# Optimization experiments

Measured on AMD Instinct MI355X. Metric: run time of the kernel, lower is better.

The kernel has to match this reference:

```python
import jax, jax.numpy as jnp
import numpy as np

BLOCK_SIZE = 32
BLOCK_COUNTS = 16
B, N, H, D = 4, 1024, 8, 64
LENGTHS = np.array([1024, 768, 512, 896], dtype=np.int64)


def setup_inputs() -> dict:
    key = jax.random.key(0)
    ks = jax.random.split(key, 8)
    offsets = np.concatenate([[0], np.cumsum(LENGTHS)]).astype(np.int32)
    mask = np.zeros((B, N), dtype=bool)
    for b in range(B):
        mask[b, : int(LENGTHS[b])] = True
    gather_idx = np.nonzero(mask.reshape(-1))[0].astype(np.int32)
    m = jnp.asarray(mask)[:, :, None, None].astype(jnp.float32)
    padded_q = jax.random.normal(ks[0], (B, N, H, D), jnp.float32) * m
    padded_k = jax.random.normal(ks[1], (B, N, H, D), jnp.float32) * m
    padded_v = jax.random.normal(ks[2], (B, N, H, D), jnp.float32) * m
    gidx = jnp.asarray(gather_idx)
    jagged_q = padded_q.reshape(B * N, H, D)[gidx]
    jagged_k = padded_k.reshape(B * N, H, D)[gidx]
    jagged_v = padded_v.reshape(B * N, H, D)[gidx]
    jagged_u = jax.random.normal(ks[3], (int(gidx.shape[0]), H, D), jnp.float32)
    gate_w = jax.random.normal(ks[4], (H, D, 3), jnp.float32) * 0.1
    return {"jagged_q": jagged_q, "jagged_k": jagged_k, "jagged_v": jagged_v,
            "jagged_u": jagged_u, "padded_q": padded_q, "padded_k": padded_k,
            "padded_v": padded_v, "x_offsets": jnp.asarray(offsets),
            "gate_w": gate_w, "padding_mask": jnp.asarray(mask),
            "gather_idx": gidx}


def _forward(jagged_q, jagged_k, jagged_v, padded_q, padded_k, padded_v,
             x_offsets, gate_w, gather_idx):
    scale = D ** -0.5
    nb = N // BLOCK_SIZE                                   # N is a multiple of BLOCK_SIZE (pad_len=0)
    S = min(BLOCK_COUNTS, nb)
    lengths = x_offsets[1:] - x_offsets[:-1]               # [B]
    cmp_len = (lengths + BLOCK_SIZE - 1) // BLOCK_SIZE     # [B] valid compressed blocks per seq
    pos = jnp.arange(N)
    blk = jnp.arange(nb)
    q_blk = pos // BLOCK_SIZE

    # scatter jagged tokens back to dense padded layout (zeros at padding) --
    # the Triton kernels read q/k/v from the jagged tensors.
    def to_dense(j):
        return jnp.zeros((B * N, H, D), j.dtype).at[gather_idx].set(j).reshape(B, N, H, D)
    qd, kd, vd = to_dense(jagged_q), to_dense(jagged_k), to_dense(jagged_v)

    # gates: per-token/per-head sigmoid linear gate from padded_q -> (g_cmp, g_slc, g_swa)
    gates = jax.nn.sigmoid(jnp.einsum('bnhd,hdg->bnhg', padded_q, gate_w))
    g_cmp, g_slc = gates[..., 0], gates[..., 1]            # g_swa unused by this module

    # compressed (block-mean) keys / values  [B, nb, H, D]
    k_cmp = padded_k.reshape(B, nb, BLOCK_SIZE, H, D).mean(axis=2)
    v_cmp = padded_v.reshape(B, nb, BLOCK_SIZE, H, D).mean(axis=2)

    # ---- compressed branch: SiLU attention over block-mean keys ----
    s_cmp = jnp.einsum('bqhd,bkhd->bqhk', qd, k_cmp) * scale          # [B,N,H,nb]
    mask_cmp = (q_blk[:, None] >= blk[None, :])[None, :, None, :] & \
               (blk[None, None, None, :] < cmp_len[:, None, None, None])
    p_cmp = jnp.where(mask_cmp, jax.nn.silu(s_cmp), 0.0)
    o_cmp = jnp.einsum('bqhk,bkhd->bqhd', p_cmp, v_cmp) * g_cmp[..., None]

    # ---- block selection: causal top-k over compressed scores ----
    s_sel = jnp.einsum('bqhd,bkhd->bhqk', padded_q, k_cmp) * scale    # [B,H,N,nb]
    causal_blk = (q_blk[:, None] >= blk[None, :])[None, None]
    _, top_idx = jax.lax.top_k(jnp.where(causal_blk, s_sel, -jnp.inf), S)  # [B,H,N,S]
    top_idx = jnp.where(top_idx > q_blk[None, None, :, None], -1, top_idx)
    top_idx = top_idx.transpose(0, 2, 1, 3)                           # [B,N,H,S]

    # ---- selected branch: SiLU attention restricted to selected blocks ----
    blk_sel = jnp.any(top_idx[..., None] == blk, axis=-2)             # [B,N,H,nb] (-1 matches nothing)
    key_sel = jnp.repeat(blk_sel, BLOCK_SIZE, axis=-1)                # [B,N,H,N]
    mask_slc = key_sel & (pos[:, None] >= pos[None, :])[None, :, None, :]
    s_slc = jnp.einsum('bqhd,bkhd->bqhk', qd, kd) * scale             # [B,N,H,N]
    p_slc = jnp.where(mask_slc, jax.nn.silu(s_slc), 0.0)
    o_slc = jnp.einsum('bqhk,bkhd->bqhd', p_slc, vd) * g_slc[..., None]

    # jagged output: gather valid tokens
    return (o_cmp + o_slc).reshape(B * N, H, D)[gather_idx]


def reference(jagged_q, jagged_k, jagged_v, jagged_u, padded_q, padded_k,
              padded_v, x_offsets, gate_w, padding_mask, gather_idx):
    return _forward(jagged_q, jagged_k, jagged_v, padded_q, padded_k,
                    padded_v, x_offsets, gate_w, gather_idx)
```

## Files before the change

kernel.cpp:

```cpp
#include <hip/hip_runtime.h>
#include <math.h>
#include <stdint.h>

#define BB 4
#define NN 1024
#define HH 8
#define DD 64
#define BS 32
#define NB 32
#define SS 16

typedef __attribute__((ext_vector_type(8)))  short bf16x8;
typedef __attribute__((ext_vector_type(16))) float f32x16;
typedef __attribute__((ext_vector_type(2)))  int   int2v;

union FragU { bf16x8 h; uint32_t u[4]; };

#define ZERO16 {0.f,0.f,0.f,0.f,0.f,0.f,0.f,0.f,0.f,0.f,0.f,0.f,0.f,0.f,0.f,0.f}

__device__ __forceinline__ uint32_t cvt_pk_bf16(float lo, float hi) {
    uint32_t r;
    asm("v_cvt_pk_bf16_f32 %0, %1, %2" : "=v"(r) : "v"(lo), "v"(hi));
    return r;
}

__device__ __forceinline__ float silu_f(float x) {
    return __fdividef(x, 1.f + __expf(-x));
}

__global__ void cmp_mean_kernel(const float* __restrict__ pk,
                                const float* __restrict__ pv,
                                float* __restrict__ kc,
                                float* __restrict__ vc) {
    int idx = blockIdx.x * 4 + (threadIdx.x >> 6);
    int d = threadIdx.x & 63;
    int h = idx & 7;
    int blk = (idx >> 3) & 31;
    int b = idx >> 8;
    size_t base = (((size_t)b * NN + (size_t)blk * BS) * HH + h) * DD + d;
    float ks = 0.f, vs = 0.f;
    #pragma unroll
    for (int j = 0; j < BS; ++j) {
        ks += pk[base + (size_t)j * HH * DD];
        vs += pv[base + (size_t)j * HH * DD];
    }
    kc[(size_t)idx * DD + d] = ks * (1.f / BS);
    vc[(size_t)idx * DD + d] = vs * (1.f / BS);
}

__global__ __launch_bounds__(256, 3) void bsa_mfma_kernel(
    const float* __restrict__ pq, const float* __restrict__ pk,
    const float* __restrict__ pv, const float* __restrict__ kc,
    const float* __restrict__ vc, const float* __restrict__ gw,
    const int* __restrict__ xoff, float* __restrict__ out)
{
    __shared__ float qlds[32][64];
    __shared__ __align__(16) uint16_t pcmp[32][40];
    __shared__ uint32_t selmask[32];
    __shared__ float gateC[32], gateS[32];
    __shared__ float olds[5][32][64];

    const int tid = threadIdx.x;
    const int lane = tid & 63;
    const int w = tid >> 6;
    const int l31 = lane & 31;
    const int hi = lane >> 5;

    const int bid = blockIdx.x;
    const int t_id = (bid & 7) * 128 + (bid >> 3);
    const int qb = t_id & 31;
    const int h = (t_id >> 5) & 7;
    const int b = t_id >> 8;

    const int off0 = xoff[b];
    const int len = xoff[b + 1] - off0;
    if (qb * BS >= len) return;

    {
        int q = tid >> 3, part = (tid & 7) * 8;
        const float* src = pq + (((size_t)(b * NN + qb * BS + q)) * HH + h) * DD + part;
        *(float4*)&qlds[q][part] = *(const float4*)src;
        *(float4*)&qlds[q][part + 4] = *(const float4*)(src + 4);
    }

    FragU qf[4];
    {
        const float* qrow = pq + (((size_t)(b * NN + qb * BS + l31)) * HH + h) * DD;
        #pragma unroll
        for (int t = 0; t < 4; ++t) {
            const float* qp = qrow + t * 16 + hi * 8;
            float4 x = *(const float4*)qp;
            float4 y = *(const float4*)(qp + 4);
            qf[t].u[0] = cvt_pk_bf16(x.x, x.y);
            qf[t].u[1] = cvt_pk_bf16(x.z, x.w);
            qf[t].u[2] = cvt_pk_bf16(y.x, y.y);
            qf[t].u[3] = cvt_pk_bf16(y.z, y.w);
        }
    }

    float4 kcv[8];
    {
        const float* kcrow = kc + (((size_t)(b * NB + l31)) * HH + h) * DD + hi * 32;
        #pragma unroll
        for (int i = 0; i < 8; ++i) kcv[i] = *(const float4*)(kcrow + i * 4);
    }

    __syncthreads();

    for (int j = 0; j < 8; ++j) {
        int q = w * 8 + j;
        const float* qv = qlds[q];
        const float* qh = qv + hi * 32;
        float part = 0.f;
        #pragma unroll
        for (int i = 0; i < 8; ++i) {
            float4 qq = *(const float4*)(qh + i * 4);
            part += qq.x * kcv[i].x + qq.y * kcv[i].y + qq.z * kcv[i].z + qq.w * kcv[i].w;
        }
        float s = (part + __shfl_xor(part, 32)) * 0.125f;
        float p = (l31 <= qb) ? silu_f(s) : 0.f;
        if (lane < 32) {
            uint32_t fb = __float_as_uint(p);
            uint16_t bp = (uint16_t)((fb + 0x7fffu + ((fb >> 16) & 1u)) >> 16);
            pcmp[q][l31] = bp;
        }
        uint32_t m;
        if (qb >= SS) {
            float vsel = (l31 <= qb) ? s : -INFINITY;
            int rank = 0;
            #pragma unroll
            for (int off = 1; off < 32; ++off) {
                float o = __shfl_xor(vsel, off);
                int oi = l31 ^ off;
                rank += (o > vsel || (o == vsel && oi < l31)) ? 1 : 0;
            }
            m = (uint32_t)(__ballot(rank < SS) & 0xffffffffu);
        } else {
            m = (1u << (qb + 1)) - 1u;
        }
        if (lane == 0) selmask[q] = m;
        float qd = qv[lane];
        float g0 = qd * gw[(h * DD + lane) * 3 + 0];
        float g1 = qd * gw[(h * DD + lane) * 3 + 1];
        #pragma unroll
        for (int off = 32; off; off >>= 1) {
            g0 += __shfl_xor(g0, off);
            g1 += __shfl_xor(g1, off);
        }
        if (lane == 0) {
            gateC[q] = __frcp_rn(1.f + __expf(-g0));
            gateS[q] = __frcp_rn(1.f + __expf(-g1));
        }
    }

    __syncthreads();

    const uint32_t mymask = selmask[l31];
    f32x16 accO0 = ZERO16, accO1 = ZERO16;

    if (w == 3) {
        f32x16 c0 = ZERO16, c1 = ZERO16;
        #pragma unroll
        for (int s = 0; s < 2; ++s) {
            FragU pa;
            pa.h = *(const bf16x8*)&pcmp[l31][s * 16 + hi * 8];
            const float* vbase = vc + (((size_t)(b * NB + s * 16 + hi * 8)) * HH + h) * DD + l31;
            #pragma unroll
            for (int dh = 0; dh < 2; ++dh) {
                FragU vb;
                #pragma unroll
                for (int jj = 0; jj < 4; ++jj) {
                    float a = vbase[(2 * jj) * 512 + dh * 32];
                    float c = vbase[(2 * jj + 1) * 512 + dh * 32];
                    vb.u[jj] = cvt_pk_bf16(a, c);
                }
                if (dh == 0) c0 = __builtin_amdgcn_mfma_f32_32x32x16_bf16(pa.h, vb.h, c0, 0, 0, 0);
                else         c1 = __builtin_amdgcn_mfma_f32_32x32x16_bf16(pa.h, vb.h, c1, 0, 0, 0);
            }
        }
        #pragma unroll
        for (int r = 0; r < 16; ++r) {
            int q = (r & 3) + 8 * (r >> 2) + 4 * hi;
            olds[4][q][l31] = c0[r];
            olds[4][q][32 + l31] = c1[r];
        }
    }

    const int qpos = qb * BS + l31;
    for (int kb = w; kb <= qb; kb += 4) {
        f32x16 accS = ZERO16;
        const float* krow = pk + (((size_t)(b * NN + kb * BS + l31)) * HH + h) * DD;
        #pragma unroll
        for (int t = 0; t < 4; ++t) {
            const float* kp = krow + t * 16 + hi * 8;
            float4 x = *(const float4*)kp;
            float4 y = *(const float4*)(kp + 4);
            FragU kf;
            kf.u[0] = cvt_pk_bf16(x.x, x.y);
            kf.u[1] = cvt_pk_bf16(x.z, x.w);
            kf.u[2] = cvt_pk_bf16(y.x, y.y);
            kf.u[3] = cvt_pk_bf16(y.z, y.w);
            accS = __builtin_amdgcn_mfma_f32_32x32x16_bf16(kf.h, qf[t].h, accS, 0, 0, 0);
        }
        const bool selbit = (mymask >> kb) & 1;
        const bool notdiag = kb < qb;
        float pr[16];
        #pragma unroll
        for (int r = 0; r < 16; ++r) {
            int key = (r & 3) + 8 * (r >> 2) + 4 * hi;
            int kpos = kb * BS + key;
            float s = accS[r] * 0.125f;
            bool ok = selbit && (notdiag || kpos <= qpos);
            pr[r] = ok ? silu_f(s) : 0.f;
        }
        uint32_t wv[8];
        #pragma unroll
        for (int i = 0; i < 8; ++i) wv[i] = cvt_pk_bf16(pr[2 * i], pr[2 * i + 1]);
        int2v e0 = __builtin_amdgcn_permlane32_swap(wv[0], wv[2], false, false);
        int2v e1 = __builtin_amdgcn_permlane32_swap(wv[1], wv[3], false, false);
        int2v e2 = __builtin_amdgcn_permlane32_swap(wv[4], wv[6], false, false);
        int2v e3 = __builtin_amdgcn_permlane32_swap(wv[5], wv[7], false, false);
        FragU a0, a1;
        a0.u[0] = e0[0]; a0.u[1] = e1[0]; a0.u[2] = e0[1]; a0.u[3] = e1[1];
        a1.u[0] = e2[0]; a1.u[1] = e3[0]; a1.u[2] = e2[1]; a1.u[3] = e3[1];
        #pragma unroll
        for (int s = 0; s < 2; ++s) {
            const float* vbase = pv + (((size_t)(b * NN + kb * BS + s * 16 + hi * 8)) * HH + h) * DD + l31;
            const FragU& pa = s ? a1 : a0;
            #pragma unroll
            for (int dh = 0; dh < 2; ++dh) {
                FragU vb;
                #pragma unroll
                for (int jj = 0; jj < 4; ++jj) {
                    float a = vbase[(2 * jj) * 512 + dh * 32];
                    float c = vbase[(2 * jj + 1) * 512 + dh * 32];
                    vb.u[jj] = cvt_pk_bf16(a, c);
                }
                if (dh == 0) accO0 = __builtin_amdgcn_mfma_f32_32x32x16_bf16(pa.h, vb.h, accO0, 0, 0, 0);
                else         accO1 = __builtin_amdgcn_mfma_f32_32x32x16_bf16(pa.h, vb.h, accO1, 0, 0, 0);
            }
        }
    }

    #pragma unroll
    for (int r = 0; r < 16; ++r) {
        int q = (r & 3) + 8 * (r >> 2) + 4 * hi;
        olds[w][q][l31] = accO0[r];
        olds[w][q][32 + l31] = accO1[r];
    }

    __syncthreads();

    {
        int q = tid >> 3, dpart = (tid & 7) * 8;
        int pos = qb * BS + q;
        if (pos < len) {
            float gc = gateC[q], gs = gateS[q];
            float res[8];
            #pragma unroll
            for (int dd = 0; dd < 8; ++dd) {
                int d = dpart + dd;
                float sum = olds[0][q][d] + olds[1][q][d] + olds[2][q][d] + olds[3][q][d];
                res[dd] = gc * olds[4][q][d] + gs * sum;
            }
            float* op = out + (((size_t)(off0 + pos)) * HH + h) * DD + dpart;
            *(float4*)op = make_float4(res[0], res[1], res[2], res[3]);
            *(float4*)(op + 4) = make_float4(res[4], res[5], res[6], res[7]);
        }
    }
}

extern "C" void kernel_launch(void* const* d_in, const int* in_sizes, int n_in,
                              void* d_out, int out_size, void* d_ws, size_t ws_size,
                              hipStream_t stream) {
    const float* pq = (const float*)d_in[4];
    const float* pk = (const float*)d_in[5];
    const float* pv = (const float*)d_in[6];
    const int* xoff = (const int*)d_in[7];
    const float* gw = (const float*)d_in[8];
    float* out = (float*)d_out;

    float* kc = (float*)d_ws;
    float* vc = kc + (size_t)BB * NB * HH * DD;

    cmp_mean_kernel<<<BB * NB * HH / 4, 256, 0, stream>>>(pk, pv, kc, vc);
    bsa_mfma_kernel<<<BB * HH * NB, 256, 0, stream>>>(pq, pk, pv, kc, vc, gw, xoff, out);
}
```

Baseline: 160.4 us.

## Iterate only over selected key blocks and reduce outputs via LDS atomics

The selected-branch loop now visits only key blocks that some query row in the tile actually selected (the union mask across rows), instead of every causal block, and spreads those blocks round-robin over the waves. Per-wave output buffers in LDS are replaced by a single buffer that is zeroed first and filled with gated atomic adds. This shrinks LDS use, which allows launch bounds of 4 blocks per CU. Block ordering is changed to stagger qb across (b,h), and the mean-pool kernel now uses float4 loads with a shuffle reduction. The risks are LDS atomic contention and uneven work per wave.

```diff
diff --git a/kernel.cpp b/kernel.cpp
--- a/kernel.cpp
+++ b/kernel.cpp
@@ -28,27 +28,42 @@
     return __fdividef(x, 1.f + __expf(-x));
 }
 
-__global__ void cmp_mean_kernel(const float* __restrict__ pk,
-                                const float* __restrict__ pv,
-                                float* __restrict__ kc,
-                                float* __restrict__ vc) {
-    int idx = blockIdx.x * 4 + (threadIdx.x >> 6);
-    int d = threadIdx.x & 63;
-    int h = idx & 7;
-    int blk = (idx >> 3) & 31;
-    int b = idx >> 8;
-    size_t base = (((size_t)b * NN + (size_t)blk * BS) * HH + h) * DD + d;
-    float ks = 0.f, vs = 0.f;
+__global__ __launch_bounds__(256) void cmp_mean_kernel(
+    const float* __restrict__ pk, const float* __restrict__ pv,
+    float* __restrict__ kc, float* __restrict__ vc)
+{
+    int w = threadIdx.x >> 6;
+    int lane = threadIdx.x & 63;
+    int idx = blockIdx.x * 4 + w;
+    int r0 = lane >> 4;
+    int c4 = (lane & 15) << 2;
+    int h = idx & 7, blk = (idx >> 3) & 31, b = idx >> 8;
+    size_t base = (((size_t)(b * NN + blk * BS + r0)) * HH + h) * DD + c4;
+    float k0=0,k1=0,k2=0,k3=0,v0=0,v1=0,v2=0,v3=0;
     #pragma unroll
-    for (int j = 0; j < BS; ++j) {
-        ks += pk[base + (size_t)j * HH * DD];
-        vs += pv[base + (size_t)j * HH * DD];
-    }
-    kc[(size_t)idx * DD + d] = ks * (1.f / BS);
-    vc[(size_t)idx * DD + d] = vs * (1.f / BS);
-}
-
-__global__ __launch_bounds__(256, 3) void bsa_mfma_kernel(
+    for (int j = 0; j < 8; ++j) {
+        const float* kp = pk + base + (size_t)j * 4 * HH * DD;
+        const float* vp = pv + base + (size_t)j * 4 * HH * DD;
+        float4 a = *(const float4*)kp;
+        float4 c = *(const float4*)vp;
+        k0+=a.x; k1+=a.y; k2+=a.z; k3+=a.w;
+        v0+=c.x; v1+=c.y; v2+=c.z; v3+=c.w;
+    }
+    #pragma unroll
+    for (int off = 16; off < 64; off <<= 1) {
+        k0 += __shfl_xor(k0, off); k1 += __shfl_xor(k1, off);
+        k2 += __shfl_xor(k2, off); k3 += __shfl_xor(k3, off);
+        v0 += __shfl_xor(v0, off); v1 += __shfl_xor(v1, off);
+        v2 += __shfl_xor(v2, off); v3 += __shfl_xor(v3, off);
+    }
+    if (lane < 16) {
+        const float sc = 1.f / BS;
+        *(float4*)(kc + (size_t)idx * DD + c4) = make_float4(k0*sc, k1*sc, k2*sc, k3*sc);
+        *(float4*)(vc + (size_t)idx * DD + c4) = make_float4(v0*sc, v1*sc, v2*sc, v3*sc);
+    }
+}
+
+__global__ __launch_bounds__(256, 4) void bsa_mfma_kernel(
     const float* __restrict__ pq, const float* __restrict__ pk,
     const float* __restrict__ pv, const float* __restrict__ kc,
     const float* __restrict__ vc, const float* __restrict__ gw,
@@ -58,7 +73,7 @@
     __shared__ __align__(16) uint16_t pcmp[32][40];
     __shared__ uint32_t selmask[32];
     __shared__ float gateC[32], gateS[32];
-    __shared__ float olds[5][32][64];
+    __shared__ float olds[32][64];
 
     const int tid = threadIdx.x;
     const int lane = tid & 63;
@@ -67,14 +82,21 @@
     const int hi = lane >> 5;
 
     const int bid = blockIdx.x;
-    const int t_id = (bid & 7) * 128 + (bid >> 3);
-    const int qb = t_id & 31;
-    const int h = (t_id >> 5) & 7;
-    const int b = t_id >> 8;
+    const int qi = bid & 31;
+    const int bh = bid >> 5;
+    const int qb = (qi + bh) & 31;
+    const int h = bh & 7;
+    const int b = bh >> 3;
 
     const int off0 = xoff[b];
     const int len = xoff[b + 1] - off0;
     if (qb * BS >= len) return;
+
+    {
+        int q = tid >> 3, d = (tid & 7) * 8;
+        *(float4*)&olds[q][d] = make_float4(0.f, 0.f, 0.f, 0.f);
+        *(float4*)&olds[q][d + 4] = make_float4(0.f, 0.f, 0.f, 0.f);
+    }
 
     {
         int q = tid >> 3, part = (tid & 7) * 8;
@@ -156,7 +178,9 @@
     __syncthreads();
 
     const uint32_t mymask = selmask[l31];
-    f32x16 accO0 = ZERO16, accO1 = ZERO16;
+    uint32_t tmask = mymask;
+    #pragma unroll
+    for (int off = 1; off < 32; off <<= 1) tmask |= __shfl_xor(tmask, off);
 
     if (w == 3) {
         f32x16 c0 = ZERO16, c1 = ZERO16;
@@ -181,72 +205,85 @@
         #pragma unroll
         for (int r = 0; r < 16; ++r) {
             int q = (r & 3) + 8 * (r >> 2) + 4 * hi;
-            olds[4][q][l31] = c0[r];
-            olds[4][q][32 + l31] = c1[r];
-        }
-    }
-
+            float gc = gateC[q];
+            atomicAdd(&olds[q][l31], gc * c0[r]);
+            atomicAdd(&olds[q][32 + l31], gc * c1[r]);
+        }
+    }
+
+    f32x16 accO0 = ZERO16, accO1 = ZERO16;
+    bool any = false;
     const int qpos = qb * BS + l31;
-    for (int kb = w; kb <= qb; kb += 4) {
-        f32x16 accS = ZERO16;
-        const float* krow = pk + (((size_t)(b * NN + kb * BS + l31)) * HH + h) * DD;
-        #pragma unroll
-        for (int t = 0; t < 4; ++t) {
-            const float* kp = krow + t * 16 + hi * 8;
-            float4 x = *(const float4*)kp;
-            float4 y = *(const float4*)(kp + 4);
-            FragU kf;
-            kf.u[0] = cvt_pk_bf16(x.x, x.y);
-            kf.u[1] = cvt_pk_bf16(x.z, x.w);
-            kf.u[2] = cvt_pk_bf16(y.x, y.y);
-            kf.u[3] = cvt_pk_bf16(y.z, y.w);
-            accS = __builtin_amdgcn_mfma_f32_32x32x16_bf16(kf.h, qf[t].h, accS, 0, 0, 0);
-        }
-        const bool selbit = (mymask >> kb) & 1;
-        const bool notdiag = kb < qb;
-        float pr[16];
+    {
+        uint32_t m = tmask;
+        int bcnt = 0;
+        while (m) {
+            int kb = __builtin_ctz(m); m &= m - 1;
+            if (((bcnt++) & 3) != w) continue;
+            any = true;
+            f32x16 accS = ZERO16;
+            const float* krow = pk + (((size_t)(b * NN + kb * BS + l31)) * HH + h) * DD;
+            #pragma unroll
+            for (int t = 0; t < 4; ++t) {
+                const float* kp = krow + t * 16 + hi * 8;
+                float4 x = *(const float4*)kp;
+                float4 y = *(const float4*)(kp + 4);
+                FragU kf;
+                kf.u[0] = cvt_pk_bf16(x.x, x.y);
+                kf.u[1] = cvt_pk_bf16(x.z, x.w);
+                kf.u[2] = cvt_pk_bf16(y.x, y.y);
+                kf.u[3] = cvt_pk_bf16(y.z, y.w);
+                accS = __builtin_amdgcn_mfma_f32_32x32x16_bf16(kf.h, qf[t].h, accS, 0, 0, 0);
+            }
+            const bool selbit = (mymask >> kb) & 1;
+            const bool notdiag = kb < qb;
+            float pr[16];
+            #pragma unroll
+            for (int r = 0; r < 16; ++r) {
+                int key = (r & 3) + 8 * (r >> 2) + 4 * hi;
+                int kpos = kb * BS + key;
+                float s = accS[r] * 0.125f;
+                bool ok = selbit && (notdiag || kpos <= qpos);
+                pr[r] = ok ? silu_f(s) : 0.f;
+            }
+            uint32_t wv[8];
+            #pragma unroll
+            for (int i = 0; i < 8; ++i) wv[i] = cvt_pk_bf16(pr[2 * i], pr[2 * i + 1]);
+            int2v e0 = __builtin_amdgcn_permlane32_swap(wv[0], wv[2], false, false);
+            int2v e1 = __builtin_amdgcn_permlane32_swap(wv[1], wv[3], false, false);
+            int2v e2 = __builtin_amdgcn_permlane32_swap(wv[4], wv[6], false, false);
+            int2v e3 = __builtin_amdgcn_permlane32_swap(wv[5], wv[7], false, false);
+            FragU a0, a1;
+            a0.u[0] = e0[0]; a0.u[1] = e1[0]; a0.u[2] = e0[1]; a0.u[3] = e1[1];
+            a1.u[0] = e2[0]; a1.u[1] = e3[0]; a1.u[2] = e2[1]; a1.u[3] = e3[1];
+            #pragma unroll
+            for (int s = 0; s < 2; ++s) {
+                const float* vbase = pv + (((size_t)(b * NN + kb * BS + s * 16 + hi * 8)) * HH + h) * DD + l31;
+                const FragU& pa = s ? a1 : a0;
+                #pragma unroll
+                for (int dh = 0; dh < 2; ++dh) {
+                    FragU vb;
+                    #pragma unroll
+                    for (int jj = 0; jj < 4; ++jj) {
+                        float a = vbase[(2 * jj) * 512 + dh * 32];
+                        float c = vbase[(2 * jj + 1) * 512 + dh * 32];
+                        vb.u[jj] = cvt_pk_bf16(a, c);
+                    }
+                    if (dh == 0) accO0 = __builtin_amdgcn_mfma_f32_32x32x16_bf16(pa.h, vb.h, accO0, 0, 0, 0);
+                    else         accO1 = __builtin_amdgcn_mfma_f32_32x32x16_bf16(pa.h, vb.h, accO1, 0, 0, 0);
+                }
+            }
+        }
+    }
+
+    if (any) {
         #pragma unroll
         for (int r = 0; r < 16; ++r) {
-            int key = (r & 3) + 8 * (r >> 2) + 4 * hi;
-            int kpos = kb * BS + key;
-            float s = accS[r] * 0.125f;
-            bool ok = selbit && (notdiag || kpos <= qpos);
-            pr[r] = ok ? silu_f(s) : 0.f;
-        }
-        uint32_t wv[8];
-        #pragma unroll
-        for (int i = 0; i < 8; ++i) wv[i] = cvt_pk_bf16(pr[2 * i], pr[2 * i + 1]);
-        int2v e0 = __builtin_amdgcn_permlane32_swap(wv[0], wv[2], false, false);
-        int2v e1 = __builtin_amdgcn_permlane32_swap(wv[1], wv[3], false, false);
-        int2v e2 = __builtin_amdgcn_permlane32_swap(wv[4], wv[6], false, false);
-        int2v e3 = __builtin_amdgcn_permlane32_swap(wv[5], wv[7], false, false);
-        FragU a0, a1;
-        a0.u[0] = e0[0]; a0.u[1] = e1[0]; a0.u[2] = e0[1]; a0.u[3] = e1[1];
-        a1.u[0] = e2[0]; a1.u[1] = e3[0]; a1.u[2] = e2[1]; a1.u[3] = e3[1];
-        #pragma unroll
-        for (int s = 0; s < 2; ++s) {
-            const float* vbase = pv + (((size_t)(b * NN + kb * BS + s * 16 + hi * 8)) * HH + h) * DD + l31;
-            const FragU& pa = s ? a1 : a0;
-            #pragma unroll
-            for (int dh = 0; dh < 2; ++dh) {
-                FragU vb;
-                #pragma unroll
-                for (int jj = 0; jj < 4; ++jj) {
-                    float a = vbase[(2 * jj) * 512 + dh * 32];
-                    float c = vbase[(2 * jj + 1) * 512 + dh * 32];
-                    vb.u[jj] = cvt_pk_bf16(a, c);
-                }
-                if (dh == 0) accO0 = __builtin_amdgcn_mfma_f32_32x32x16_bf16(pa.h, vb.h, accO0, 0, 0, 0);
-                else         accO1 = __builtin_amdgcn_mfma_f32_32x32x16_bf16(pa.h, vb.h, accO1, 0, 0, 0);
-            }
-        }
-    }
-
-    #pragma unroll
-    for (int r = 0; r < 16; ++r) {
-        int q = (r & 3) + 8 * (r >> 2) + 4 * hi;
-        olds[w][q][l31] = accO0[r];
-        olds[w][q][32 + l31] = accO1[r];
+            int q = (r & 3) + 8 * (r >> 2) + 4 * hi;
+            float gs = gateS[q];
+            atomicAdd(&olds[q][l31], gs * accO0[r]);
+            atomicAdd(&olds[q][32 + l31], gs * accO1[r]);
+        }
     }
 
     __syncthreads();
@@ -255,17 +292,9 @@
         int q = tid >> 3, dpart = (tid & 7) * 8;
         int pos = qb * BS + q;
         if (pos < len) {
-            float gc = gateC[q], gs = gateS[q];
-            float res[8];
-            #pragma unroll
-            for (int dd = 0; dd < 8; ++dd) {
-                int d = dpart + dd;
-                float sum = olds[0][q][d] + olds[1][q][d] + olds[2][q][d] + olds[3][q][d];
-                res[dd] = gc * olds[4][q][d] + gs * sum;
-            }
             float* op = out + (((size_t)(off0 + pos)) * HH + h) * DD + dpart;
-            *(float4*)op = make_float4(res[0], res[1], res[2], res[3]);
-            *(float4*)(op + 4) = make_float4(res[4], res[5], res[6], res[7]);
+            *(float4*)op = *(float4*)&olds[q][dpart];
+            *(float4*)(op + 4) = *(float4*)&olds[q][dpart + 4];
         }
     }
 }
```

Measured after the change: 184.6 us. 15.1% more time.
